# Performance work log

Measured on AMD Instinct MI355X. Metric: run time of the kernel, lower is better.

The kernel has to match this reference:

```python
import jax, jax.numpy as jnp
import numpy as np

B, T, D = 32, 1024, 1024
PCA_DIM = 256
NS = 4
NC = 1024
SEC = PCA_DIM // NS


def setup_inputs() -> dict:
    key = jax.random.key(0)
    k1, k2, k3 = jax.random.split(key, 3)
    inputs = jax.random.normal(k1, (B, T, D), dtype=jnp.float32)
    # variance_scaling(1.0, 'fan_avg', 'normal'): std = sqrt(2 / (fan_in + fan_out))
    pca_proj = jax.random.normal(k2, (D, PCA_DIM), dtype=jnp.float32) * np.float32(np.sqrt(2.0 / (D + PCA_DIM)))
    pre_bias = jnp.zeros((1, D), dtype=jnp.float32)
    # per-section codebooks, variance_scaling(0.1, 'fan_avg', 'normal')
    codebooks = jax.random.normal(k3, (NS, NC, SEC), dtype=jnp.float32) * np.float32(np.sqrt(0.1 * 2.0 / (NC + SEC)))
    return {"inputs": inputs, "pca_proj": pca_proj, "pre_bias": pre_bias, "codebooks": codebooks}


def reference(inputs, pca_proj, pre_bias, codebooks):
    in_shape = inputs.shape
    d = in_shape[-1]
    flat = inputs.reshape(-1, d)  # [N, D]
    n = flat.shape[0]
    # --- PCA projection + reconstruction / decorrelation losses ---
    projected = (flat + pre_bias) @ pca_proj            # [N, P]
    unprojected = projected @ pca_proj.T - pre_bias     # [N, D]
    l2_loss = jnp.mean(jnp.sqrt(jnp.sum(jnp.square(flat - unprojected), axis=-1)))
    cov = projected.T @ projected / n                   # [P, P]
    cov_loss = jnp.mean(jnp.square(cov - jnp.eye(pca_proj.shape[1], dtype=projected.dtype)))
    pca_loss = l2_loss + cov_loss
    # --- per-section vector quantization ---
    ns, nc, sec = codebooks.shape
    secs = projected.reshape(n, ns, sec).transpose(1, 0, 2)  # [ns, N, sec] == jnp.split along -1

    def quantize_section(x, cb):
        # x: [N, sec], cb: [nc, sec]; squared-L2 cdist via expansion
        dist = (jnp.sum(x * x, axis=1, keepdims=True)
                - 2.0 * (x @ cb.T)
                + jnp.sum(cb * cb, axis=1)[None, :])    # [N, nc]
        idx = jnp.argmin(dist, axis=1)                  # [N]
        q = cb[idx]                                     # gather == one_hot @ cb
        loss = jnp.square(q - jax.lax.stop_gradient(x))  # [N, sec]
        q_st = x + jax.lax.stop_gradient(q - x)         # straight-through
        return q_st, loss, idx

    q, sec_loss, idx = jax.vmap(quantize_section)(secs, codebooks)  # [ns,N,sec] x2, [ns,N]
    quantized = q.transpose(1, 0, 2).reshape(n, ns * sec)           # concat sections -> [N, P]
    quantized = (quantized @ pca_proj.T - pre_bias).reshape(in_shape)  # pca_unproject
    nn_idx = idx.reshape((ns,) + in_shape[:-1])                     # [ns, B, T]
    quantization_loss = jnp.mean(sec_loss.reshape((ns,) + in_shape[:-1] + (sec,)), axis=0) + pca_loss
    codebook = jax.lax.stop_gradient(codebooks.reshape(ns * nc, sec))
    cluster_counts = jnp.ones((ns, nc), dtype=jnp.float32)  # eval mode: jnp.ones init, no EMA
    return quantized, quantization_loss, nn_idx, codebook, cluster_counts
```

## Files before the change

kernel.cpp:

```cpp
#include <hip/hip_runtime.h>
#include <math.h>

#define NROW 32768
#define DIM  1024
#define PDIM 256
#define NSEC 4
#define NCODE 1024
#define SECD 64

__global__ __launch_bounds__(256) void k_proj(const float* __restrict__ X,
                                              const float* __restrict__ W,
                                              const float* __restrict__ bias,
                                              float* __restrict__ proj) {
    __shared__ float As[16][128];
    __shared__ float Bs[16][128];
    const int t = threadIdx.x;
    const int ry = t >> 4;
    const int rx = t & 15;
    const int rb = blockIdx.y * 128;
    const int cb = blockIdx.x * 128;
    const int lr = t >> 1;
    const int lk = (t & 1) * 8;
    const int bk = t >> 4;
    const int bc = (t & 15) * 8;
    float acc[8][8] = {};
    float part[8][8] = {};
    for (int kc = 0; kc < DIM; kc += 16) {
        if (kc == 384) {
            #pragma unroll
            for (int i = 0; i < 8; ++i)
                #pragma unroll
                for (int j = 0; j < 8; ++j) { part[i][j] = acc[i][j]; acc[i][j] = 0.0f; }
        } else if (kc == 768) {
            #pragma unroll
            for (int i = 0; i < 8; ++i)
                #pragma unroll
                for (int j = 0; j < 8; ++j) { part[i][j] = __fadd_rn(part[i][j], acc[i][j]); acc[i][j] = 0.0f; }
        }
        float4 a0 = *(const float4*)&X[(size_t)(rb + lr) * DIM + kc + lk];
        float4 a1 = *(const float4*)&X[(size_t)(rb + lr) * DIM + kc + lk + 4];
        float4 c0 = *(const float4*)&bias[kc + lk];
        float4 c1 = *(const float4*)&bias[kc + lk + 4];
        a0.x += c0.x; a0.y += c0.y; a0.z += c0.z; a0.w += c0.w;
        a1.x += c1.x; a1.y += c1.y; a1.z += c1.z; a1.w += c1.w;
        float4 b0 = *(const float4*)&W[(size_t)(kc + bk) * PDIM + cb + bc];
        float4 b1 = *(const float4*)&W[(size_t)(kc + bk) * PDIM + cb + bc + 4];
        As[lk + 0][lr] = a0.x; As[lk + 1][lr] = a0.y; As[lk + 2][lr] = a0.z; As[lk + 3][lr] = a0.w;
        As[lk + 4][lr] = a1.x; As[lk + 5][lr] = a1.y; As[lk + 6][lr] = a1.z; As[lk + 7][lr] = a1.w;
        *(float4*)&Bs[bk][bc] = b0;
        *(float4*)&Bs[bk][bc + 4] = b1;
        __syncthreads();
        #pragma unroll
        for (int k = 0; k < 16; ++k) {
            float4 x0 = *(const float4*)&As[k][ry * 8];
            float4 x1 = *(const float4*)&As[k][ry * 8 + 4];
            float4 y0 = *(const float4*)&Bs[k][rx * 8];
            float4 y1 = *(const float4*)&Bs[k][rx * 8 + 4];
            float aa[8] = {x0.x, x0.y, x0.z, x0.w, x1.x, x1.y, x1.z, x1.w};
            float bb[8] = {y0.x, y0.y, y0.z, y0.w, y1.x, y1.y, y1.z, y1.w};
            #pragma unroll
            for (int i = 0; i < 8; ++i)
                #pragma unroll
                for (int j = 0; j < 8; ++j)
                    acc[i][j] = fmaf(aa[i], bb[j], acc[i][j]);
        }
        __syncthreads();
    }
    #pragma unroll
    for (int i = 0; i < 8; ++i) {
        float r[8];
        #pragma unroll
        for (int j = 0; j < 8; ++j) r[j] = __fadd_rn(part[i][j], acc[i][j]);
        const size_t base = (size_t)(rb + ry * 8 + i) * PDIM + cb + rx * 8;
        *(float4*)&proj[base]     = make_float4(r[0], r[1], r[2], r[3]);
        *(float4*)&proj[base + 4] = make_float4(r[4], r[5], r[6], r[7]);
    }
}

__global__ __launch_bounds__(256) void k_pm(const float* __restrict__ P,
                                            const float* __restrict__ M,
                                            float* __restrict__ PM) {
    __shared__ float As[16][128];
    __shared__ float Bs[16][128];
    const int t = threadIdx.x;
    const int ry = t >> 4;
    const int rx = t & 15;
    const int rb = blockIdx.y * 128;
    const int cb = blockIdx.x * 128;
    const int lr = t >> 1;
    const int lk = (t & 1) * 8;
    const int bk = t >> 4;
    const int bc = (t & 15) * 8;
    float acc[8][8] = {};
    for (int kc = 0; kc < PDIM; kc += 16) {
        float4 a0 = *(const float4*)&P[(size_t)(rb + lr) * PDIM + kc + lk];
        float4 a1 = *(const float4*)&P[(size_t)(rb + lr) * PDIM + kc + lk + 4];
        float4 b0 = *(const float4*)&M[(size_t)(kc + bk) * PDIM + cb + bc];
        float4 b1 = *(const float4*)&M[(size_t)(kc + bk) * PDIM + cb + bc + 4];
        As[lk + 0][lr] = a0.x; As[lk + 1][lr] = a0.y; As[lk + 2][lr] = a0.z; As[lk + 3][lr] = a0.w;
        As[lk + 4][lr] = a1.x; As[lk + 5][lr] = a1.y; As[lk + 6][lr] = a1.z; As[lk + 7][lr] = a1.w;
        *(float4*)&Bs[bk][bc] = b0;
        *(float4*)&Bs[bk][bc + 4] = b1;
        __syncthreads();
        #pragma unroll
        for (int k = 0; k < 16; ++k) {
            float4 x0 = *(const float4*)&As[k][ry * 8];
            float4 x1 = *(const float4*)&As[k][ry * 8 + 4];
            float4 y0 = *(const float4*)&Bs[k][rx * 8];
            float4 y1 = *(const float4*)&Bs[k][rx * 8 + 4];
            float aa[8] = {x0.x, x0.y, x0.z, x0.w, x1.x, x1.y, x1.z, x1.w};
            float bb[8] = {y0.x, y0.y, y0.z, y0.w, y1.x, y1.y, y1.z, y1.w};
            #pragma unroll
            for (int i = 0; i < 8; ++i)
                #pragma unroll
                for (int j = 0; j < 8; ++j)
                    acc[i][j] = fmaf(aa[i], bb[j], acc[i][j]);
        }
        __syncthreads();
    }
    #pragma unroll
    for (int i = 0; i < 8; ++i) {
        const size_t base = (size_t)(rb + ry * 8 + i) * PDIM + cb + rx * 8;
        *(float4*)&PM[base]     = make_float4(acc[i][0], acc[i][1], acc[i][2], acc[i][3]);
        *(float4*)&PM[base + 4] = make_float4(acc[i][4], acc[i][5], acc[i][6], acc[i][7]);
    }
}

__global__ __launch_bounds__(256) void k_wtw(const float* __restrict__ W,
                                             float* __restrict__ M) {
    __shared__ float As[16][64];
    __shared__ float Bs[16][64];
    const int t = threadIdx.x;
    const int tx = t & 15, ty = t >> 4;
    const int ib = blockIdx.x * 64;
    const int jb = blockIdx.y * 64;
    const int sk = t >> 4;
    const int sc = (t & 15) * 4;
    float acc[4][4] = {};
    for (int kc = 0; kc < DIM; kc += 16) {
        float4 a = *(const float4*)&W[(size_t)(kc + sk) * PDIM + ib + sc];
        float4 b = *(const float4*)&W[(size_t)(kc + sk) * PDIM + jb + sc];
        *(float4*)&As[sk][sc] = a;
        *(float4*)&Bs[sk][sc] = b;
        __syncthreads();
        #pragma unroll
        for (int k = 0; k < 16; ++k) {
            float4 a4 = *(const float4*)&As[k][ty * 4];
            float4 b4 = *(const float4*)&Bs[k][tx * 4];
            float aa[4] = {a4.x, a4.y, a4.z, a4.w};
            float bb[4] = {b4.x, b4.y, b4.z, b4.w};
            #pragma unroll
            for (int i = 0; i < 4; ++i)
                #pragma unroll
                for (int j = 0; j < 4; ++j)
                    acc[i][j] = fmaf(aa[i], bb[j], acc[i][j]);
        }
        __syncthreads();
    }
    #pragma unroll
    for (int i = 0; i < 4; ++i)
        #pragma unroll
        for (int j = 0; j < 4; ++j)
            M[(size_t)(ib + ty * 4 + i) * PDIM + jb + tx * 4 + j] = acc[i][j];
}

__global__ __launch_bounds__(256) void k_xn2(const float* __restrict__ X,
                                             const float* __restrict__ bias,
                                             float* __restrict__ xn2) {
    const int n = blockIdx.x * 4 + (threadIdx.x >> 6);
    const int lane = threadIdx.x & 63;
    float s = 0.0f;
    #pragma unroll
    for (int i = 0; i < 4; ++i) {
        float4 x = *(const float4*)&X[(size_t)n * DIM + i * 256 + lane * 4];
        float4 b = *(const float4*)&bias[i * 256 + lane * 4];
        float vx = x.x + b.x, vy = x.y + b.y, vz = x.z + b.z, vw = x.w + b.w;
        s = fmaf(vx, vx, s); s = fmaf(vy, vy, s);
        s = fmaf(vz, vz, s); s = fmaf(vw, vw, s);
    }
    #pragma unroll
    for (int o = 1; o < 64; o <<= 1) s += __shfl_xor(s, o);
    if (lane == 0) xn2[n] = s;
}

__global__ __launch_bounds__(256) void k_rowres(const float* __restrict__ P,
                                                const float* __restrict__ PM,
                                                const float* __restrict__ xn2,
                                                float* __restrict__ rowres) {
    const int n = blockIdx.x * 4 + (threadIdx.x >> 6);
    const int lane = threadIdx.x & 63;
    float4 p  = *(const float4*)&P[(size_t)n * PDIM + lane * 4];
    float4 pm = *(const float4*)&PM[(size_t)n * PDIM + lane * 4];
    float s = 0.0f;
    s = fmaf(p.x, pm.x - 2.0f * p.x, s);
    s = fmaf(p.y, pm.y - 2.0f * p.y, s);
    s = fmaf(p.z, pm.z - 2.0f * p.z, s);
    s = fmaf(p.w, pm.w - 2.0f * p.w, s);
    #pragma unroll
    for (int o = 1; o < 64; o <<= 1) s += __shfl_xor(s, o);
    if (lane == 0) rowres[n] = xn2[n] + s;
}

__global__ __launch_bounds__(256) void k_cov(const float* __restrict__ Pm,
                                             float* __restrict__ cov) {
    __shared__ float As[16][64];
    __shared__ float Bs[16][64];
    const int t = threadIdx.x;
    const int tx = t & 15, ty = t >> 4;
    const int ib = blockIdx.x * 64;
    const int jb = blockIdx.y * 64;
    const int nb = blockIdx.z * 2048;
    const int sk = t >> 4;
    const int sc = (t & 15) * 4;
    float acc[4][4] = {};
    for (int kc = 0; kc < 2048; kc += 16) {
        float4 a = *(const float4*)&Pm[(size_t)(nb + kc + sk) * PDIM + ib + sc];
        float4 b = *(const float4*)&Pm[(size_t)(nb + kc + sk) * PDIM + jb + sc];
        *(float4*)&As[sk][sc] = a;
        *(float4*)&Bs[sk][sc] = b;
        __syncthreads();
        #pragma unroll
        for (int k = 0; k < 16; ++k) {
            float4 a4 = *(const float4*)&As[k][ty * 4];
            float4 b4 = *(const float4*)&Bs[k][tx * 4];
            float aa[4] = {a4.x, a4.y, a4.z, a4.w};
            float bb[4] = {b4.x, b4.y, b4.z, b4.w};
            #pragma unroll
            for (int i = 0; i < 4; ++i)
                #pragma unroll
                for (int j = 0; j < 4; ++j)
                    acc[i][j] = fmaf(aa[i], bb[j], acc[i][j]);
        }
        __syncthreads();
    }
    #pragma unroll
    for (int i = 0; i < 4; ++i)
        #pragma unroll
        for (int j = 0; j < 4; ++j)
            atomicAdd(&cov[(size_t)(ib + ty * 4 + i) * PDIM + jb + tx * 4 + j], acc[i][j]);
}

__global__ __launch_bounds__(256) void k_covloss(const float* __restrict__ cov,
                                                 float* __restrict__ scal) {
    const int t = threadIdx.x;
    float s = 0.0f;
    for (int e = t; e < PDIM * PDIM; e += 256) {
        int i = e >> 8, j = e & 255;
        float v = cov[e] * (1.0f / 32768.0f) - (i == j ? 1.0f : 0.0f);
        s = fmaf(v, v, s);
    }
    #pragma unroll
    for (int o = 1; o < 64; o <<= 1) s += __shfl_xor(s, o);
    __shared__ float r4[4];
    if ((t & 63) == 0) r4[t >> 6] = s;
    __syncthreads();
    if (t == 0) scal[1] = (r4[0] + r4[1] + r4[2] + r4[3]) * (1.0f / 65536.0f);
}

__global__ __launch_bounds__(256) void k_l2(const float* __restrict__ rowres,
                                            float* __restrict__ scal) {
    int r = blockIdx.x * 256 + threadIdx.x;
    float v = sqrtf(rowres[r]);
    #pragma unroll
    for (int o = 1; o < 64; o <<= 1) v += __shfl_xor(v, o);
    if ((threadIdx.x & 63) == 0) atomicAdd(&scal[0], v);
}

__global__ __launch_bounds__(256) void k_cnorm(const float* __restrict__ cbs,
                                               float* __restrict__ cnorm) {
    int c = blockIdx.x * 256 + threadIdx.x;
    const float* p = &cbs[(size_t)c * SECD];
    float a[8];
    #pragma unroll
    for (int j = 0; j < 8; ++j) a[j] = __fmul_rn(p[j], p[j]);
    #pragma unroll
    for (int i = 8; i < 64; i += 8)
        #pragma unroll
        for (int j = 0; j < 8; ++j)
            a[j] = __fadd_rn(a[j], __fmul_rn(p[i + j], p[i + j]));
    float r = __fadd_rn(__fadd_rn(__fadd_rn(a[0], a[1]), __fadd_rn(a[2], a[3])),
                        __fadd_rn(__fadd_rn(a[4], a[5]), __fadd_rn(a[6], a[7])));
    cnorm[c] = r;
}

__global__ __launch_bounds__(256) void k_vq(const float* __restrict__ proj,
                                            const float* __restrict__ cbs,
                                            const float* __restrict__ cnorm,
                                            int* __restrict__ widx,
                                            float* __restrict__ out_idx,
                                            float* __restrict__ out_qloss) {
    __shared__ float xs[64][64];
    __shared__ float cs[64][128];
    __shared__ float xnorm[64];
    __shared__ int   sidx[64];
    const int t = threadIdx.x;
    const int ry = t >> 5;
    const int tx = t & 31;
    const int rb = blockIdx.x * 64;
    const int lr = t >> 2;
    const int kq = (t & 3) * 16;
    const int cr = t >> 1;
    const int ko = (t & 1) * 32;
    float qacc[16];
    #pragma unroll
    for (int i = 0; i < 16; ++i) qacc[i] = 0.0f;

    for (int s = 0; s < NSEC; ++s) {
        #pragma unroll
        for (int i = 0; i < 16; i += 4) {
            float4 v = *(const float4*)&proj[(size_t)(rb + lr) * PDIM + s * SECD + kq + i];
            xs[kq + i + 0][lr] = v.x; xs[kq + i + 1][lr] = v.y;
            xs[kq + i + 2][lr] = v.z; xs[kq + i + 3][lr] = v.w;
        }
        __syncthreads();
        if (t < 64) {
            float a[8];
            #pragma unroll
            for (int j = 0; j < 8; ++j) { float v = xs[j][t]; a[j] = __fmul_rn(v, v); }
            #pragma unroll
            for (int i = 8; i < 64; i += 8)
                #pragma unroll
                for (int j = 0; j < 8; ++j) {
                    float v = xs[i + j][t];
                    a[j] = __fadd_rn(a[j], __fmul_rn(v, v));
                }
            xnorm[t] = __fadd_rn(__fadd_rn(__fadd_rn(a[0], a[1]), __fadd_rn(a[2], a[3])),
                                 __fadd_rn(__fadd_rn(a[4], a[5]), __fadd_rn(a[6], a[7])));
        }
        float best[8]; int bidx[8];
        #pragma unroll
        for (int i = 0; i < 8; ++i) { best[i] = 3.4e38f; bidx[i] = 0; }

        for (int ct = 0; ct < 8; ++ct) {
            __syncthreads();
            #pragma unroll
            for (int u = 0; u < 32; u += 4) {
                float4 v = *(const float4*)&cbs[(size_t)(s * NCODE + ct * 128 + cr) * SECD + ko + u];
                cs[ko + u + 0][cr] = v.x; cs[ko + u + 1][cr] = v.y;
                cs[ko + u + 2][cr] = v.z; cs[ko + u + 3][cr] = v.w;
            }
            __syncthreads();
            float4 cn4 = *(const float4*)&cnorm[s * NCODE + ct * 128 + tx * 4];
            float cna[4] = {cn4.x, cn4.y, cn4.z, cn4.w};
            float acc[8][4] = {};
            #pragma unroll 8
            for (int k = 0; k < 64; ++k) {
                float4 x0 = *(const float4*)&xs[k][ry * 8];
                float4 x1 = *(const float4*)&xs[k][ry * 8 + 4];
                float4 b4 = *(const float4*)&cs[k][tx * 4];
                float aa[8] = {x0.x, x0.y, x0.z, x0.w, x1.x, x1.y, x1.z, x1.w};
                float bb[4] = {b4.x, b4.y, b4.z, b4.w};
                #pragma unroll
                for (int i = 0; i < 8; ++i)
                    #pragma unroll
                    for (int j = 0; j < 4; ++j)
                        acc[i][j] = fmaf(aa[i], bb[j], acc[i][j]);
            }
            #pragma unroll
            for (int i = 0; i < 8; ++i) {
                float xn = xnorm[ry * 8 + i];
                #pragma unroll
                for (int j = 0; j < 4; ++j) {
                    float d = __fadd_rn(__fsub_rn(xn, __fmul_rn(2.0f, acc[i][j])), cna[j]);
                    int code = ct * 128 + tx * 4 + j;
                    if (d < best[i]) { best[i] = d; bidx[i] = code; }
                }
            }
        }
        #pragma unroll
        for (int i = 0; i < 8; ++i) {
            float d = best[i]; int ix = bidx[i];
            #pragma unroll
            for (int o = 1; o < 32; o <<= 1) {
                float od = __shfl_xor(d, o);
                int   oi = __shfl_xor(ix, o);
                if (od < d || (od == d && oi < ix)) { d = od; ix = oi; }
            }
            if (tx == 0) {
                int row = rb + ry * 8 + i;
                widx[s * NROW + row] = ix;
                out_idx[s * NROW + row] = (float)ix;
                sidx[ry * 8 + i] = ix;
            }
        }
        __syncthreads();
        {
            const float* crow = &cbs[(size_t)(s * NCODE + sidx[lr]) * SECD];
            #pragma unroll
            for (int i = 0; i < 16; i += 4) {
                float4 q = *(const float4*)&crow[kq + i];
                float qq[4] = {q.x, q.y, q.z, q.w};
                #pragma unroll
                for (int u = 0; u < 4; ++u) {
                    float d = qq[u] - xs[kq + i + u][lr];
                    qacc[i + u] = fmaf(d, d, qacc[i + u]);
                }
            }
        }
        __syncthreads();
    }
    #pragma unroll
    for (int i = 0; i < 16; i += 4) {
        float4 v = make_float4(0.25f * qacc[i + 0], 0.25f * qacc[i + 1],
                               0.25f * qacc[i + 2], 0.25f * qacc[i + 3]);
        *(float4*)&out_qloss[(size_t)(rb + lr) * SECD + kq + i] = v;
    }
}

__global__ __launch_bounds__(256) void k_cbu(const float* __restrict__ cbs,
                                             const float* __restrict__ W,
                                             float* __restrict__ cbu) {
    __shared__ float As[16][64];
    __shared__ float Bs[16][64];
    const int t = threadIdx.x;
    const int tx = t & 15, ty = t >> 4;
    const int s = blockIdx.z;
    const int cbase = blockIdx.y * 64;
    const int db = blockIdx.x * 64;
    const int lr = t >> 2;
    const int lk = (t & 3) * 4;
    float acc[4][4] = {};
    for (int kc = 0; kc < SECD; kc += 16) {
        float4 a = *(const float4*)&cbs[(size_t)(s * NCODE + cbase + lr) * SECD + kc + lk];
        float4 b = *(const float4*)&W[(size_t)(db + lr) * PDIM + s * SECD + kc + lk];
        As[lk + 0][lr] = a.x; As[lk + 1][lr] = a.y;
        As[lk + 2][lr] = a.z; As[lk + 3][lr] = a.w;
        Bs[lk + 0][lr] = b.x; Bs[lk + 1][lr] = b.y;
        Bs[lk + 2][lr] = b.z; Bs[lk + 3][lr] = b.w;
        __syncthreads();
        #pragma unroll
        for (int k = 0; k < 16; ++k) {
            float4 a4 = *(const float4*)&As[k][ty * 4];
            float4 b4 = *(const float4*)&Bs[k][tx * 4];
            float aa[4] = {a4.x, a4.y, a4.z, a4.w};
            float bb[4] = {b4.x, b4.y, b4.z, b4.w};
            #pragma unroll
            for (int i = 0; i < 4; ++i)
                #pragma unroll
                for (int j = 0; j < 4; ++j)
                    acc[i][j] = fmaf(aa[i], bb[j], acc[i][j]);
        }
        __syncthreads();
    }
    #pragma unroll
    for (int i = 0; i < 4; ++i) {
        float4 v = make_float4(acc[i][0], acc[i][1], acc[i][2], acc[i][3]);
        *(float4*)&cbu[(size_t)(s * NCODE + cbase + ty * 4 + i) * DIM + db + tx * 4] = v;
    }
}

__global__ __launch_bounds__(256) void k_gather(const float* __restrict__ cbu,
                                                const int* __restrict__ widx,
                                                const float* __restrict__ bias,
                                                float* __restrict__ out0) {
    const int n = blockIdx.x;
    const int d = threadIdx.x * 4;
    int i0 = widx[0 * NROW + n];
    int i1 = widx[1 * NROW + n];
    int i2 = widx[2 * NROW + n];
    int i3 = widx[3 * NROW + n];
    float4 v0 = *(const float4*)&cbu[((size_t)(0 * NCODE + i0)) * DIM + d];
    float4 v1 = *(const float4*)&cbu[((size_t)(1 * NCODE + i1)) * DIM + d];
    float4 v2 = *(const float4*)&cbu[((size_t)(2 * NCODE + i2)) * DIM + d];
    float4 v3 = *(const float4*)&cbu[((size_t)(3 * NCODE + i3)) * DIM + d];
    float4 b = *(const float4*)&bias[d];
    float4 r;
    r.x = v0.x + v1.x + v2.x + v3.x - b.x;
    r.y = v0.y + v1.y + v2.y + v3.y - b.y;
    r.z = v0.z + v1.z + v2.z + v3.z - b.z;
    r.w = v0.w + v1.w + v2.w + v3.w - b.w;
    *(float4*)&out0[(size_t)n * DIM + d] = r;
}

__global__ __launch_bounds__(256) void k_addpca(float* __restrict__ out1,
                                                const float* __restrict__ scal) {
    float pca = scal[0] * (1.0f / 32768.0f) + scal[1];
    int e = blockIdx.x * 256 + threadIdx.x;
    float4* p = (float4*)out1;
    float4 v = p[e];
    v.x += pca; v.y += pca; v.z += pca; v.w += pca;
    p[e] = v;
}

__global__ __launch_bounds__(256) void k_tail(const float* __restrict__ cbs,
                                              float* __restrict__ out3,
                                              float* __restrict__ out4) {
    int e = blockIdx.x * 256 + threadIdx.x;
    ((float4*)out3)[e] = ((const float4*)cbs)[e];
    if (e < 4096) out4[e] = 1.0f;
}

extern "C" void kernel_launch(void* const* d_in, const int* in_sizes, int n_in,
                              void* d_out, int out_size, void* d_ws, size_t ws_size,
                              hipStream_t stream) {
    (void)in_sizes; (void)n_in; (void)out_size; (void)ws_size;
    const float* X    = (const float*)d_in[0];
    const float* W    = (const float*)d_in[1];
    const float* bias = (const float*)d_in[2];
    const float* cbs  = (const float*)d_in[3];

    float* out  = (float*)d_out;
    float* out0 = out;
    float* out1 = out + 33554432;
    float* out2 = out + 35651584;
    float* out3 = out + 35782656;
    float* out4 = out + 36044800;

    char* ws = (char*)d_ws;
    float* cbu    = (float*)(ws);
    float* rowres = (float*)(ws + 16777216);
    float* cov    = (float*)(ws + 16908288);
    float* scal   = (float*)(ws + 17170432);
    float* cnorm  = (float*)(ws + 17170496);
    int*   widx   = (int*)  (ws + 17186880);
    float* wtw    = (float*)(ws + 17711168);

    float* proj = out0;
    float* PM   = out0 + 16777216;
    float* xn2  = out0 + 25165824;

    hipMemsetAsync(ws + 16908288, 0, 262144 + 64, stream);

    k_proj    <<<dim3(2, 256),    256, 0, stream>>>(X, W, bias, proj);
    k_xn2     <<<8192,            256, 0, stream>>>(X, bias, xn2);
    k_wtw     <<<dim3(4, 4),      256, 0, stream>>>(W, wtw);
    k_cov     <<<dim3(4, 4, 16),  256, 0, stream>>>(proj, cov);
    k_covloss <<<1,               256, 0, stream>>>(cov, scal);
    k_pm      <<<dim3(2, 256),    256, 0, stream>>>(proj, wtw, PM);
    k_rowres  <<<8192,            256, 0, stream>>>(proj, PM, xn2, rowres);
    k_l2      <<<128,             256, 0, stream>>>(rowres, scal);
    k_cnorm   <<<16,              256, 0, stream>>>(cbs, cnorm);
    k_vq      <<<512,             256, 0, stream>>>(proj, cbs, cnorm, widx, out2, out1);
    k_cbu     <<<dim3(16, 16, 4), 256, 0, stream>>>(cbs, W, cbu);
    k_gather  <<<32768,           256, 0, stream>>>(cbu, widx, bias, out0);
    k_addpca  <<<2048,            256, 0, stream>>>(out1, scal);
    k_tail    <<<256,             256, 0, stream>>>(cbs, out3, out4);
}
```

Before: 1.266 ms.

## Split-K the projection and PM GEMMs with direct-to-LDS loads of W

```diff
diff --git a/kernel.cpp b/kernel.cpp
--- a/kernel.cpp
+++ b/kernel.cpp
@@ -8,54 +8,48 @@
 #define NCODE 1024
 #define SECD 64
 
-__global__ __launch_bounds__(256) void k_proj(const float* __restrict__ X,
-                                              const float* __restrict__ W,
-                                              const float* __restrict__ bias,
-                                              float* __restrict__ proj) {
-    __shared__ float As[16][128];
-    __shared__ float Bs[16][128];
-    const int t = threadIdx.x;
-    const int ry = t >> 4;
-    const int rx = t & 15;
-    const int rb = blockIdx.y * 128;
-    const int cb = blockIdx.x * 128;
-    const int lr = t >> 1;
-    const int lk = (t & 1) * 8;
-    const int bk = t >> 4;
-    const int bc = (t & 15) * 8;
+__global__ __launch_bounds__(256, 4) void k_proj(const float* __restrict__ X,
+                                                 const float* __restrict__ W,
+                                                 const float* __restrict__ bias,
+                                                 float* __restrict__ p0) {
+    __shared__ __align__(16) float As[16][68];
+    __shared__ __align__(16) float Bs[16][256];
+    const int t  = threadIdx.x;
+    const int ry = t >> 5;
+    const int rx = t & 31;
+    const int rb = blockIdx.x * 64;
+    const int z  = blockIdx.z;
+    const int k0 = z * 384;
+    const int kn = (z == 2) ? 256 : 384;
+    const int lr = t >> 2;
+    const int ks = (t & 3) * 4;
+    const int wv = t >> 6;
+    const int ln = t & 63;
+    const int gsw = ((ln & 31) << 1) | (ln >> 5);
+    float* outp = p0 + (size_t)z * ((size_t)NROW * PDIM);
     float acc[8][8] = {};
-    float part[8][8] = {};
-    for (int kc = 0; kc < DIM; kc += 16) {
-        if (kc == 384) {
-            #pragma unroll
-            for (int i = 0; i < 8; ++i)
-                #pragma unroll
-                for (int j = 0; j < 8; ++j) { part[i][j] = acc[i][j]; acc[i][j] = 0.0f; }
-        } else if (kc == 768) {
-            #pragma unroll
-            for (int i = 0; i < 8; ++i)
-                #pragma unroll
-                for (int j = 0; j < 8; ++j) { part[i][j] = __fadd_rn(part[i][j], acc[i][j]); acc[i][j] = 0.0f; }
-        }
-        float4 a0 = *(const float4*)&X[(size_t)(rb + lr) * DIM + kc + lk];
-        float4 a1 = *(const float4*)&X[(size_t)(rb + lr) * DIM + kc + lk + 4];
-        float4 c0 = *(const float4*)&bias[kc + lk];
-        float4 c1 = *(const float4*)&bias[kc + lk + 4];
-        a0.x += c0.x; a0.y += c0.y; a0.z += c0.z; a0.w += c0.w;
-        a1.x += c1.x; a1.y += c1.y; a1.z += c1.z; a1.w += c1.w;
-        float4 b0 = *(const float4*)&W[(size_t)(kc + bk) * PDIM + cb + bc];
-        float4 b1 = *(const float4*)&W[(size_t)(kc + bk) * PDIM + cb + bc + 4];
-        As[lk + 0][lr] = a0.x; As[lk + 1][lr] = a0.y; As[lk + 2][lr] = a0.z; As[lk + 3][lr] = a0.w;
-        As[lk + 4][lr] = a1.x; As[lk + 5][lr] = a1.y; As[lk + 6][lr] = a1.z; As[lk + 7][lr] = a1.w;
-        *(float4*)&Bs[bk][bc] = b0;
-        *(float4*)&Bs[bk][bc + 4] = b1;
+    for (int kc = k0; kc < k0 + kn; kc += 16) {
+        #pragma unroll
+        for (int j = 0; j < 4; ++j) {
+            const int krow = wv * 4 + j;
+            __builtin_amdgcn_global_load_lds(
+                (const __attribute__((address_space(1))) void*)(W + (size_t)(kc + krow) * PDIM + gsw * 4),
+                (__attribute__((address_space(3))) void*)(&Bs[krow][0]),
+                16, 0, 0);
+        }
+        float4 a = *(const float4*)&X[(size_t)(rb + lr) * DIM + kc + ks];
+        float4 c = *(const float4*)&bias[kc + ks];
+        As[ks + 0][lr] = a.x + c.x;
+        As[ks + 1][lr] = a.y + c.y;
+        As[ks + 2][lr] = a.z + c.z;
+        As[ks + 3][lr] = a.w + c.w;
         __syncthreads();
         #pragma unroll
         for (int k = 0; k < 16; ++k) {
             float4 x0 = *(const float4*)&As[k][ry * 8];
             float4 x1 = *(const float4*)&As[k][ry * 8 + 4];
-            float4 y0 = *(const float4*)&Bs[k][rx * 8];
-            float4 y1 = *(const float4*)&Bs[k][rx * 8 + 4];
+            float4 y0 = *(const float4*)&Bs[k][rx * 4];
+            float4 y1 = *(const float4*)&Bs[k][128 + rx * 4];
             float aa[8] = {x0.x, x0.y, x0.z, x0.w, x1.x, x1.y, x1.z, x1.w};
             float bb[8] = {y0.x, y0.y, y0.z, y0.w, y1.x, y1.y, y1.z, y1.w};
             #pragma unroll
@@ -68,46 +62,65 @@
     }
     #pragma unroll
     for (int i = 0; i < 8; ++i) {
-        float r[8];
-        #pragma unroll
-        for (int j = 0; j < 8; ++j) r[j] = __fadd_rn(part[i][j], acc[i][j]);
-        const size_t base = (size_t)(rb + ry * 8 + i) * PDIM + cb + rx * 8;
-        *(float4*)&proj[base]     = make_float4(r[0], r[1], r[2], r[3]);
-        *(float4*)&proj[base + 4] = make_float4(r[4], r[5], r[6], r[7]);
-    }
-}
-
-__global__ __launch_bounds__(256) void k_pm(const float* __restrict__ P,
-                                            const float* __restrict__ M,
-                                            float* __restrict__ PM) {
-    __shared__ float As[16][128];
-    __shared__ float Bs[16][128];
-    const int t = threadIdx.x;
-    const int ry = t >> 4;
-    const int rx = t & 15;
-    const int rb = blockIdx.y * 128;
-    const int cb = blockIdx.x * 128;
-    const int lr = t >> 1;
-    const int lk = (t & 1) * 8;
-    const int bk = t >> 4;
-    const int bc = (t & 15) * 8;
+        const size_t base = (size_t)(rb + ry * 8 + i) * PDIM + rx * 8;
+        *(float4*)&outp[base]     = make_float4(acc[i][0], acc[i][1], acc[i][2], acc[i][3]);
+        *(float4*)&outp[base + 4] = make_float4(acc[i][4], acc[i][5], acc[i][6], acc[i][7]);
+    }
+}
+
+__global__ __launch_bounds__(256) void k_comb(float* __restrict__ p) {
+    const size_t i = ((size_t)blockIdx.x * 256 + threadIdx.x) * 4;
+    float4 a = *(const float4*)&p[i];
+    float4 b = *(const float4*)&p[i + 8388608];
+    float4 c = *(const float4*)&p[i + 16777216];
+    float4 r;
+    r.x = __fadd_rn(__fadd_rn(a.x, b.x), c.x);
+    r.y = __fadd_rn(__fadd_rn(a.y, b.y), c.y);
+    r.z = __fadd_rn(__fadd_rn(a.z, b.z), c.z);
+    r.w = __fadd_rn(__fadd_rn(a.w, b.w), c.w);
+    *(float4*)&p[i] = r;
+}
+
+__global__ __launch_bounds__(256, 4) void k_pm(const float* __restrict__ P,
+                                               const float* __restrict__ M,
+                                               float* __restrict__ PMa,
+                                               float* __restrict__ PMb) {
+    __shared__ __align__(16) float As[16][68];
+    __shared__ __align__(16) float Bs[16][256];
+    const int t  = threadIdx.x;
+    const int ry = t >> 5;
+    const int rx = t & 31;
+    const int rb = blockIdx.x * 64;
+    const int z  = blockIdx.z;
+    const int k0 = z * 128;
+    const int lr = t >> 2;
+    const int ks = (t & 3) * 4;
+    const int wv = t >> 6;
+    const int ln = t & 63;
+    const int gsw = ((ln & 31) << 1) | (ln >> 5);
+    float* outp = z ? PMb : PMa;
     float acc[8][8] = {};
-    for (int kc = 0; kc < PDIM; kc += 16) {
-        float4 a0 = *(const float4*)&P[(size_t)(rb + lr) * PDIM + kc + lk];
-        float4 a1 = *(const float4*)&P[(size_t)(rb + lr) * PDIM + kc + lk + 4];
-        float4 b0 = *(const float4*)&M[(size_t)(kc + bk) * PDIM + cb + bc];
-        float4 b1 = *(const float4*)&M[(size_t)(kc + bk) * PDIM + cb + bc + 4];
-        As[lk + 0][lr] = a0.x; As[lk + 1][lr] = a0.y; As[lk + 2][lr] = a0.z; As[lk + 3][lr] = a0.w;
-        As[lk + 4][lr] = a1.x; As[lk + 5][lr] = a1.y; As[lk + 6][lr] = a1.z; As[lk + 7][lr] = a1.w;
-        *(float4*)&Bs[bk][bc] = b0;
-        *(float4*)&Bs[bk][bc + 4] = b1;
+    for (int kc = k0; kc < k0 + 128; kc += 16) {
+        #pragma unroll
+        for (int j = 0; j < 4; ++j) {
+            const int krow = wv * 4 + j;
+            __builtin_amdgcn_global_load_lds(
+                (const __attribute__((address_space(1))) void*)(M + (size_t)(kc + krow) * PDIM + gsw * 4),
+                (__attribute__((address_space(3))) void*)(&Bs[krow][0]),
+                16, 0, 0);
+        }
+        float4 a = *(const float4*)&P[(size_t)(rb + lr) * PDIM + kc + ks];
+        As[ks + 0][lr] = a.x;
+        As[ks + 1][lr] = a.y;
+        As[ks + 2][lr] = a.z;
+        As[ks + 3][lr] = a.w;
         __syncthreads();
         #pragma unroll
         for (int k = 0; k < 16; ++k) {
             float4 x0 = *(const float4*)&As[k][ry * 8];
             float4 x1 = *(const float4*)&As[k][ry * 8 + 4];
-            float4 y0 = *(const float4*)&Bs[k][rx * 8];
-            float4 y1 = *(const float4*)&Bs[k][rx * 8 + 4];
+            float4 y0 = *(const float4*)&Bs[k][rx * 4];
+            float4 y1 = *(const float4*)&Bs[k][128 + rx * 4];
             float aa[8] = {x0.x, x0.y, x0.z, x0.w, x1.x, x1.y, x1.z, x1.w};
             float bb[8] = {y0.x, y0.y, y0.z, y0.w, y1.x, y1.y, y1.z, y1.w};
             #pragma unroll
@@ -120,9 +133,9 @@
     }
     #pragma unroll
     for (int i = 0; i < 8; ++i) {
-        const size_t base = (size_t)(rb + ry * 8 + i) * PDIM + cb + rx * 8;
-        *(float4*)&PM[base]     = make_float4(acc[i][0], acc[i][1], acc[i][2], acc[i][3]);
-        *(float4*)&PM[base + 4] = make_float4(acc[i][4], acc[i][5], acc[i][6], acc[i][7]);
+        const size_t base = (size_t)(rb + ry * 8 + i) * PDIM + rx * 8;
+        *(float4*)&outp[base]     = make_float4(acc[i][0], acc[i][1], acc[i][2], acc[i][3]);
+        *(float4*)&outp[base + 4] = make_float4(acc[i][4], acc[i][5], acc[i][6], acc[i][7]);
     }
 }
 
@@ -184,18 +197,20 @@
 }
 
 __global__ __launch_bounds__(256) void k_rowres(const float* __restrict__ P,
-                                                const float* __restrict__ PM,
+                                                const float* __restrict__ PMa,
+                                                const float* __restrict__ PMb,
                                                 const float* __restrict__ xn2,
                                                 float* __restrict__ rowres) {
     const int n = blockIdx.x * 4 + (threadIdx.x >> 6);
     const int lane = threadIdx.x & 63;
     float4 p  = *(const float4*)&P[(size_t)n * PDIM + lane * 4];
-    float4 pm = *(const float4*)&PM[(size_t)n * PDIM + lane * 4];
+    float4 pa = *(const float4*)&PMa[(size_t)n * PDIM + lane * 4];
+    float4 pb = *(const float4*)&PMb[(size_t)n * PDIM + lane * 4];
     float s = 0.0f;
-    s = fmaf(p.x, pm.x - 2.0f * p.x, s);
-    s = fmaf(p.y, pm.y - 2.0f * p.y, s);
-    s = fmaf(p.z, pm.z - 2.0f * p.z, s);
-    s = fmaf(p.w, pm.w - 2.0f * p.w, s);
+    s = fmaf(p.x, (pa.x + pb.x) - 2.0f * p.x, s);
+    s = fmaf(p.y, (pa.y + pb.y) - 2.0f * p.y, s);
+    s = fmaf(p.z, (pa.z + pb.z) - 2.0f * p.z, s);
+    s = fmaf(p.w, (pa.w + pb.w) - 2.0f * p.w, s);
     #pragma unroll
     for (int o = 1; o < 64; o <<= 1) s += __shfl_xor(s, o);
     if (lane == 0) rowres[n] = xn2[n] + s;
@@ -516,18 +531,20 @@
     float* wtw    = (float*)(ws + 17711168);
 
     float* proj = out0;
-    float* PM   = out0 + 16777216;
-    float* xn2  = out0 + 25165824;
+    float* PMa  = out0 + 8388608;
+    float* PMb  = out0 + 25165824;
+    float* xn2  = out1;
 
     hipMemsetAsync(ws + 16908288, 0, 262144 + 64, stream);
 
-    k_proj    <<<dim3(2, 256),    256, 0, stream>>>(X, W, bias, proj);
+    k_proj    <<<dim3(512, 1, 3), 256, 0, stream>>>(X, W, bias, proj);
+    k_comb    <<<8192,            256, 0, stream>>>(proj);
     k_xn2     <<<8192,            256, 0, stream>>>(X, bias, xn2);
     k_wtw     <<<dim3(4, 4),      256, 0, stream>>>(W, wtw);
     k_cov     <<<dim3(4, 4, 16),  256, 0, stream>>>(proj, cov);
     k_covloss <<<1,               256, 0, stream>>>(cov, scal);
-    k_pm      <<<dim3(2, 256),    256, 0, stream>>>(proj, wtw, PM);
-    k_rowres  <<<8192,            256, 0, stream>>>(proj, PM, xn2, rowres);
+    k_pm      <<<dim3(512, 1, 2), 256, 0, stream>>>(proj, wtw, PMa, PMb);
+    k_rowres  <<<8192,            256, 0, stream>>>(proj, PMa, PMb, xn2, rowres);
     k_l2      <<<128,             256, 0, stream>>>(rowres, scal);
     k_cnorm   <<<16,              256, 0, stream>>>(cbs, cnorm);
     k_vq      <<<512,             256, 0, stream>>>(proj, cbs, cnorm, widx, out2, out1);
```

Result: faster. 1.084 ms (-14.3%).
